# Kernel tuning notes

Hardware: AMD Instinct MI355X
Metric: run time of the kernel (lower is better)

Reference implementation:

```python
import jax, jax.numpy as jnp
import numpy as np
from jax import lax

H_STARLET = jnp.array([1/16, 1/4, 3/8, 1/4, 1/16], dtype=jnp.float32)
N_SCALES = 4

def _wav_filter():
    # outer product of the 1D starlet filter -> [5,5,1,1] HWIO
    f = jnp.outer(H_STARLET, H_STARLET)
    return f[:, :, None, None]

def _analysis(image, filt, n_scales):
    """Undecimated starlet analysis: per scale, symmetric-pad, dilated conv,
    subtract. Returns list of high-freq coeffs (each same shape as image)."""
    low = image
    coeffs = []
    half = H_STARLET.shape[0] // 2  # len(filter)//2 == 2
    for i_scale in range(n_scales):
        dil = 2 ** i_scale
        p = half * dil
        padded = jnp.pad(low, ((0, 0), (p, p), (p, p), (0, 0)), mode='symmetric')
        new_low = lax.conv_general_dilated(
            padded, filt, window_strides=(1, 1), padding='VALID',
            rhs_dilation=(dil, dil),
            dimension_numbers=('NHWC', 'HWIO', 'NHWC'))
        coeffs.append(low - new_low)
        low = new_low
    return coeffs, low

def setup_inputs() -> dict:
    key = jax.random.key(0)
    k_img, k_noise = jax.random.split(key)
    image = jax.random.normal(k_img, (16, 1024, 1024, 1), dtype=jnp.float32)
    # Replicate __init__ normalization: std of each wavelet coeff of white noise.
    filt = _wav_filter()
    noise = jax.random.normal(k_noise, (1, 1024, 1024, 1), dtype=jnp.float32)
    noise_coeffs, _ = _analysis(noise, filt, N_SCALES)
    wav_norms = jnp.stack([jnp.std(c) for c in noise_coeffs])  # [n_scales]
    return {"image": image, "wav_norms": wav_norms}

def reference(image, wav_norms):
    filt = _wav_filter()
    coeffs, _ = _analysis(image, filt, N_SCALES)
    coeffs = [c / wav_norms[i] for i, c in enumerate(coeffs)]
    # coarse=False: only the n_scales high-frequency bands are returned.
    # All have identical shape (undecimated) -> stack: [n_scales, B, H, W, 1]
    return jnp.stack(coeffs)
```

## Files before the change

### kernel.cpp

```cpp
#include <hip/hip_runtime.h>


#define IMG    1024
#define NBATCH 16
#define TILE   64
#define RTOT   30
#define SA     (TILE + 2 * RTOT)
#define BS     1024

static_assert(SA == 124, "halo arithmetic");

__device__ __forceinline__ int mirror_idx(int g, int n) {
    g = (g < 0) ? (-1 - g) : g;
    g = (g >= n) ? (2 * n - 1 - g) : g;
    return g;
}

__device__ __forceinline__ float4 tap5(float4 q0, float4 q1, float4 q2,
                                       float4 q3, float4 q4) {
    float4 o;
    o.x = 0.375f * q2.x + 0.25f * (q1.x + q3.x) + 0.0625f * (q0.x + q4.x);
    o.y = 0.375f * q2.y + 0.25f * (q1.y + q3.y) + 0.0625f * (q0.y + q4.y);
    o.z = 0.375f * q2.z + 0.25f * (q1.z + q3.z) + 0.0625f * (q0.z + q4.z);
    o.w = 0.375f * q2.w + 0.25f * (q1.w + q3.w) + 0.0625f * (q0.w + q4.w);
    return o;
}

template <int D, int NIN>
__device__ __forceinline__ void h_pass(const float* __restrict__ A,
                                       float* __restrict__ B, int tid) {
    constexpr int NOUT = NIN - 4 * D;
    constexpr int GX = NOUT / 4;
    for (int t = tid; t < NIN * GX; t += BS) {
        const int y = t / GX;
        const int x = (t - y * GX) * 4;
        const float* row = &A[y * SA + x];
        float4 o;
        if constexpr (D == 1) {
            const float4 a = *(const float4*)(row);
            const float4 b = *(const float4*)(row + 4);
            o = tap5(a,
                     make_float4(a.y, a.z, a.w, b.x),
                     make_float4(a.z, a.w, b.x, b.y),
                     make_float4(a.w, b.x, b.y, b.z),
                     b);
        } else if constexpr (D == 2) {
            const float4 a = *(const float4*)(row);
            const float4 b = *(const float4*)(row + 4);
            const float4 c = *(const float4*)(row + 8);
            o = tap5(a,
                     make_float4(a.z, a.w, b.x, b.y),
                     b,
                     make_float4(b.z, b.w, c.x, c.y),
                     c);
        } else {
            o = tap5(*(const float4*)(row),
                     *(const float4*)(row + D),
                     *(const float4*)(row + 2 * D),
                     *(const float4*)(row + 3 * D),
                     *(const float4*)(row + 4 * D));
        }
        *(float4*)(&B[y * NOUT + x]) = o;
    }
}

template <int NIN>
__device__ __forceinline__ void copy_central(const float* __restrict__ A,
                                             float* __restrict__ S, int tid) {
    constexpr int PMIN = (NIN - TILE) / 2;
    for (int t = tid; t < TILE * TILE; t += BS) {
        const int sy = t >> 6;
        const int sx = t & (TILE - 1);
        S[t] = A[(PMIN + sy) * SA + (PMIN + sx)];
    }
}

template <int D, int NIN, bool LAST>
__device__ __forceinline__ void v_pass(float* __restrict__ A,
                                       const float* __restrict__ B,
                                       const float* __restrict__ S,
                                       float* __restrict__ gout, size_t img_off,
                                       int ty0, int tx0, float inv, int tid) {
    constexpr int NOUT = NIN - 4 * D;
    constexpr int GX = NOUT / 4;
    constexpr int CMIN = (NOUT - TILE) / 2;
    for (int t = tid; t < NOUT * GX; t += BS) {
        const int y = t / GX;
        const int x = (t - y * GX) * 4;
        const float* col = &B[y * NOUT + x];
        const float4 nl = tap5(*(const float4*)(col),
                               *(const float4*)(col + D * NOUT),
                               *(const float4*)(col + 2 * D * NOUT),
                               *(const float4*)(col + 3 * D * NOUT),
                               *(const float4*)(col + 4 * D * NOUT));
        if constexpr (!LAST) {
            *(float4*)(&A[y * SA + x]) = nl;
        }
        if (y >= CMIN && y < CMIN + TILE && x >= CMIN && x < CMIN + TILE) {
            const int sy = y - CMIN, sx = x - CMIN;
            const float4 lo = *(const float4*)(&S[sy * TILE + sx]);
            float4 cf;
            cf.x = (lo.x - nl.x) * inv;
            cf.y = (lo.y - nl.y) * inv;
            cf.z = (lo.z - nl.z) * inv;
            cf.w = (lo.w - nl.w) * inv;
            *(float4*)(&gout[img_off + (size_t)(ty0 + sy) * IMG + (tx0 + sx)]) = cf;
        }
    }
}

__global__ __launch_bounds__(BS)
void starlet_fused(const float* __restrict__ img, const float* __restrict__ norms,
                   float* __restrict__ out)
{
    __shared__ float A[SA * SA];
    __shared__ float B[SA * (SA - 4)];
    __shared__ float S[TILE * TILE];

    const int tid = threadIdx.x;
    const int tx0 = blockIdx.x * TILE;
    const int ty0 = blockIdx.y * TILE;
    const size_t img_off = (size_t)blockIdx.z * (size_t)(IMG * IMG);
    const size_t plane = (size_t)NBATCH * IMG * IMG;

    const float i0 = 1.0f / norms[0];
    const float i1 = 1.0f / norms[1];
    const float i2 = 1.0f / norms[2];
    const float i3 = 1.0f / norms[3];

    for (int i = tid; i < SA * SA; i += BS) {
        const int ry = i / SA;
        const int rx = i - ry * SA;
        const int gy = mirror_idx(ty0 - RTOT + ry, IMG);
        const int gx = mirror_idx(tx0 - RTOT + rx, IMG);
        A[i] = img[img_off + (size_t)gy * IMG + gx];
    }
    __syncthreads();

    h_pass<1, 124>(A, B, tid);
    copy_central<124>(A, S, tid);
    __syncthreads();
    v_pass<1, 124, false>(A, B, S, out, img_off, ty0, tx0, i0, tid);
    __syncthreads();

    h_pass<2, 120>(A, B, tid);
    copy_central<120>(A, S, tid);
    __syncthreads();
    v_pass<2, 120, false>(A, B, S, out + plane, img_off, ty0, tx0, i1, tid);
    __syncthreads();

    h_pass<4, 112>(A, B, tid);
    copy_central<112>(A, S, tid);
    __syncthreads();
    v_pass<4, 112, false>(A, B, S, out + 2 * plane, img_off, ty0, tx0, i2, tid);
    __syncthreads();

    h_pass<8, 96>(A, B, tid);
    copy_central<96>(A, S, tid);
    __syncthreads();
    v_pass<8, 96, true>(A, B, S, out + 3 * plane, img_off, ty0, tx0, i3, tid);
}

extern "C" void kernel_launch(void* const* d_in, const int* in_sizes, int n_in,
                              void* d_out, int out_size, void* d_ws, size_t ws_size,
                              hipStream_t stream) {
    const float* image = (const float*)d_in[0];
    const float* norms = (const float*)d_in[1];
    float* out = (float*)d_out;

    dim3 grid(IMG / TILE, IMG / TILE, NBATCH);
    starlet_fused<<<grid, dim3(BS), 0, stream>>>(image, norms, out);
}
```

Baseline: 453.8 us.

## Register-chain vertical pass, vectorize central copy and interior tile loads

The vertical pass is restructured so each thread walks a column chain of 8 outputs with a sliding 5-row register window. Each row is then loaded from shared memory about 1.5 times instead of 5 times. The central-copy step now uses float4/float2 vector accesses, and interior tiles load their halo with float2 global reads that skip mirror indexing. The changes add register pressure and fewer work items per loop, and boundary tiles keep the scalar mirrored path.

```diff
diff --git a/kernel.cpp b/kernel.cpp
--- a/kernel.cpp
+++ b/kernel.cpp
@@ -68,10 +68,19 @@
 __device__ __forceinline__ void copy_central(const float* __restrict__ A,
                                              float* __restrict__ S, int tid) {
     constexpr int PMIN = (NIN - TILE) / 2;
-    for (int t = tid; t < TILE * TILE; t += BS) {
-        const int sy = t >> 6;
-        const int sx = t & (TILE - 1);
-        S[t] = A[(PMIN + sy) * SA + (PMIN + sx)];
+    for (int t = tid; t < TILE * TILE / 4; t += BS) {
+        const int sy = t >> 4;
+        const int sx = (t & 15) << 2;
+        const float* p = &A[(PMIN + sy) * SA + PMIN + sx];
+        float4 v;
+        if constexpr ((PMIN & 3) != 0) {
+            const float2 a = *(const float2*)(p);
+            const float2 b = *(const float2*)(p + 2);
+            v = make_float4(a.x, a.y, b.x, b.y);
+        } else {
+            v = *(const float4*)(p);
+        }
+        *(float4*)(&S[sy * TILE + sx]) = v;
     }
 }
 
@@ -82,29 +91,43 @@
                                        float* __restrict__ gout, size_t img_off,
                                        int ty0, int tx0, float inv, int tid) {
     constexpr int NOUT = NIN - 4 * D;
-    constexpr int GX = NOUT / 4;
+    constexpr int NQ = NOUT / 4;
+    constexpr int GY = NOUT / 8;
     constexpr int CMIN = (NOUT - TILE) / 2;
-    for (int t = tid; t < NOUT * GX; t += BS) {
-        const int y = t / GX;
-        const int x = (t - y * GX) * 4;
-        const float* col = &B[y * NOUT + x];
-        const float4 nl = tap5(*(const float4*)(col),
-                               *(const float4*)(col + D * NOUT),
-                               *(const float4*)(col + 2 * D * NOUT),
-                               *(const float4*)(col + 3 * D * NOUT),
-                               *(const float4*)(col + 4 * D * NOUT));
-        if constexpr (!LAST) {
-            *(float4*)(&A[y * SA + x]) = nl;
-        }
-        if (y >= CMIN && y < CMIN + TILE && x >= CMIN && x < CMIN + TILE) {
-            const int sy = y - CMIN, sx = x - CMIN;
-            const float4 lo = *(const float4*)(&S[sy * TILE + sx]);
-            float4 cf;
-            cf.x = (lo.x - nl.x) * inv;
-            cf.y = (lo.y - nl.y) * inv;
-            cf.z = (lo.z - nl.z) * inv;
-            cf.w = (lo.w - nl.w) * inv;
-            *(float4*)(&gout[img_off + (size_t)(ty0 + sy) * IMG + (tx0 + sx)]) = cf;
+    static_assert(NOUT % (8 * D) == 0, "chain segmentation");
+    for (int t = tid; t < NQ * GY; t += BS) {
+        const int xq = t % NQ;
+        const int g  = t / NQ;
+        const int c  = g % D;
+        const int m  = g / D;
+        const int y0 = c + 8 * D * m;
+        const int x4 = 4 * xq;
+        const bool xin = (x4 >= CMIN) && (x4 < CMIN + TILE);
+        const int sx = x4 - CMIN;
+        const float* bp = &B[y0 * NOUT + x4];
+        float4 w0, w1, w2, w3;
+        #pragma unroll
+        for (int k = 0; k < 12; ++k) {
+            const float4 r = *(const float4*)(bp + k * D * NOUT);
+            if (k >= 4) {
+                const float4 nl = tap5(w0, w1, w2, w3, r);
+                const int y = y0 + (k - 4) * D;
+                if constexpr (!LAST) {
+                    *(float4*)(&A[y * SA + x4]) = nl;
+                }
+                if (xin && y >= CMIN && y < CMIN + TILE) {
+                    const int sy = y - CMIN;
+                    const float4 lo = *(const float4*)(&S[sy * TILE + sx]);
+                    float4 cf;
+                    cf.x = (lo.x - nl.x) * inv;
+                    cf.y = (lo.y - nl.y) * inv;
+                    cf.z = (lo.z - nl.z) * inv;
+                    cf.w = (lo.w - nl.w) * inv;
+                    *(float4*)(&gout[img_off + (size_t)(ty0 + sy) * IMG +
+                                     (tx0 + sx)]) = cf;
+                }
+            }
+            w0 = w1; w1 = w2; w2 = w3; w3 = r;
         }
     }
 }
@@ -128,12 +151,24 @@
     const float i2 = 1.0f / norms[2];
     const float i3 = 1.0f / norms[3];
 
-    for (int i = tid; i < SA * SA; i += BS) {
-        const int ry = i / SA;
-        const int rx = i - ry * SA;
-        const int gy = mirror_idx(ty0 - RTOT + ry, IMG);
-        const int gx = mirror_idx(tx0 - RTOT + rx, IMG);
-        A[i] = img[img_off + (size_t)gy * IMG + gx];
+    const bool interior = (blockIdx.x >= 1) && (blockIdx.x <= 14) &&
+                          (blockIdx.y >= 1) && (blockIdx.y <= 14);
+    if (interior) {
+        const float* src = img + img_off + (size_t)(ty0 - RTOT) * IMG + (tx0 - RTOT);
+        for (int t = tid; t < SA * SA / 2; t += BS) {
+            const int ry  = t / (SA / 2);
+            const int rx2 = (t - ry * (SA / 2)) * 2;
+            const float2 v = *(const float2*)(src + (size_t)ry * IMG + rx2);
+            *(float2*)(&A[ry * SA + rx2]) = v;
+        }
+    } else {
+        for (int i = tid; i < SA * SA; i += BS) {
+            const int ry = i / SA;
+            const int rx = i - ry * SA;
+            const int gy = mirror_idx(ty0 - RTOT + ry, IMG);
+            const int gx = mirror_idx(tx0 - RTOT + rx, IMG);
+            A[i] = img[img_off + (size_t)gy * IMG + gx];
+        }
     }
     __syncthreads();
 
```

Measured after the change: 462.5 us. About the same (+1.9%).
